# Optimization experiments

Measured on AMD Instinct MI355X. Metric: run time of the kernel, lower is better.

The kernel has to match this reference:

```python
import jax, jax.numpy as jnp
import numpy as np

B, L, D, H = 32, 1024, 1024, 1024

def setup_inputs() -> dict:
    key = jax.random.key(0)
    k1, k2, k3 = jax.random.split(key, 3)
    query = jax.random.normal(k1, (B, L, D), dtype=jnp.float32)
    keys = jax.random.normal(k2, (B, L, D), dtype=jnp.float32)
    # xavier_normal for Linear(D, H): std = sqrt(2/(D+H))
    W = jax.random.normal(k3, (H, D), dtype=jnp.float32) * np.sqrt(2.0 / (D + H)).astype(np.float32)
    b = jnp.zeros((H,), dtype=jnp.float32)
    return {"query": query, "keys": keys, "W": W, "b": b}

def reference(query, keys, W, b):
    # L2-normalize along feature dim (matches torch .norm(dim=-1, keepdim=True))
    qn = query / jnp.linalg.norm(query, axis=-1, keepdims=True)
    kn = keys / jnp.linalg.norm(keys, axis=-1, keepdims=True)
    # scores[b,i,j] = <kn[b,i], qn[b,j]>  ->  [B, Lk, Lq]
    scores = jnp.einsum('bid,bjd->bij', kn, qn)
    attn = jax.nn.softmax(scores, axis=-1)
    # bmm(attn, keys) then sum over batch -> [L, D]
    out = jnp.einsum('bij,bjd->id', attn, keys)
    x = jax.nn.relu(out @ W.T + b)
    return (x, attn)
```

## Files before the change

kernel.cpp:

```cpp
#include <hip/hip_runtime.h>
#include <hip/hip_bf16.h>

#define NBATCH 32
#define Ls 1024
#define Ds 1024
#define Hs 1024

typedef float f32x4 __attribute__((ext_vector_type(4)));
typedef __bf16 v8bf __attribute__((ext_vector_type(8)));
typedef unsigned short u16x8 __attribute__((ext_vector_type(8)));
typedef unsigned short u16x4 __attribute__((ext_vector_type(4)));
typedef __hip_bfloat16 bf16;

__device__ __forceinline__ float bfbits2f(unsigned short h) {
  unsigned u = ((unsigned)h) << 16;
  return __builtin_bit_cast(float, u);
}
__device__ __forceinline__ unsigned short f2b(float x) {
  return __builtin_bit_cast(unsigned short, __float2bfloat16(x));
}
__device__ __forceinline__ u16x8 pack8(const float4& a, const float4& b, float s) {
  u16x8 r;
  r[0] = f2b(a.x * s); r[1] = f2b(a.y * s); r[2] = f2b(a.z * s); r[3] = f2b(a.w * s);
  r[4] = f2b(b.x * s); r[5] = f2b(b.y * s); r[6] = f2b(b.z * s); r[7] = f2b(b.w * s);
  return r;
}

__global__ __launch_bounds__(256) void k_convq(const float* __restrict__ q,
                                               bf16* __restrict__ qn) {
  const int w0 = ((int)blockIdx.x * 256 + (int)threadIdx.x) >> 6;
  const int lane = threadIdx.x & 63;
  #pragma unroll
  for (int it = 0; it < 2; ++it) {
    const size_t r0 = ((size_t)(it * 8192 + w0)) * 2;
    const float4* q0 = reinterpret_cast<const float4*>(q + r0 * Ds);
    float4 qv[2][4];
    #pragma unroll
    for (int rr = 0; rr < 2; ++rr)
      #pragma unroll
      for (int h = 0; h < 2; ++h) {
        qv[rr][h * 2 + 0] = q0[rr * 256 + h * 128 + lane * 2 + 0];
        qv[rr][h * 2 + 1] = q0[rr * 256 + h * 128 + lane * 2 + 1];
      }
    float sq0 = 0.f, sq1 = 0.f;
    #pragma unroll
    for (int p = 0; p < 4; ++p) {
      sq0 += qv[0][p].x*qv[0][p].x + qv[0][p].y*qv[0][p].y + qv[0][p].z*qv[0][p].z + qv[0][p].w*qv[0][p].w;
      sq1 += qv[1][p].x*qv[1][p].x + qv[1][p].y*qv[1][p].y + qv[1][p].z*qv[1][p].z + qv[1][p].w*qv[1][p].w;
    }
    #pragma unroll
    for (int o = 1; o < 64; o <<= 1) { sq0 += __shfl_xor(sq0, o); sq1 += __shfl_xor(sq1, o); }
    const float iq0 = 1.0f / sqrtf(sq0), iq1 = 1.0f / sqrtf(sq1);
    u16x8* qo = reinterpret_cast<u16x8*>(qn + r0 * Ds);
    qo[lane]        = pack8(qv[0][0], qv[0][1], iq0);
    qo[64 + lane]   = pack8(qv[0][2], qv[0][3], iq0);
    qo[128 + lane]  = pack8(qv[1][0], qv[1][1], iq1);
    qo[192 + lane]  = pack8(qv[1][2], qv[1][3], iq1);
  }
}

__global__ __launch_bounds__(256) void k_convkT(const float* __restrict__ k,
                                                bf16* __restrict__ kb,
                                                bf16* __restrict__ kT,
                                                float* __restrict__ invk) {
  __shared__ float tile[64][65];
  __shared__ float red[4][16][16];
  const int b = blockIdx.y;
  const int j0 = blockIdx.x * 64;
  const int t = threadIdx.x;
  const int jr = t >> 4;
  const int cg = t & 15;
  const int c4 = cg * 4;
  const float* src = k + (size_t)b * Ls * Ds + (size_t)j0 * Ds;
  bf16* kbd = kb + (size_t)b * Ls * Ds + (size_t)j0 * Ds;
  bf16* kTd = kT + (size_t)b * Ds * Ls + j0;
  float ssq[4] = {0.f, 0.f, 0.f, 0.f};

  for (int dc = 0; dc < 16; ++dc) {
    const int d0 = dc * 64;
    float4 v[4];
    #pragma unroll
    for (int rr = 0; rr < 4; ++rr) {
      const int j = jr + rr * 16;
      v[rr] = *reinterpret_cast<const float4*>(&src[(size_t)j * Ds + d0 + c4]);
      ssq[rr] += v[rr].x*v[rr].x + v[rr].y*v[rr].y + v[rr].z*v[rr].z + v[rr].w*v[rr].w;
      u16x4 o = { f2b(v[rr].x), f2b(v[rr].y), f2b(v[rr].z), f2b(v[rr].w) };
      *reinterpret_cast<u16x4*>(&kbd[(size_t)j * Ds + d0 + c4]) = o;
    }
    __syncthreads();
    #pragma unroll
    for (int rr = 0; rr < 4; ++rr) {
      const int j = jr + rr * 16;
      tile[j][c4 + 0] = v[rr].x; tile[j][c4 + 1] = v[rr].y;
      tile[j][c4 + 2] = v[rr].z; tile[j][c4 + 3] = v[rr].w;
    }
    __syncthreads();
    #pragma unroll
    for (int rr = 0; rr < 4; ++rr) {
      const int dd = jr + rr * 16;
      u16x4 o = { f2b(tile[c4 + 0][dd]), f2b(tile[c4 + 1][dd]),
                  f2b(tile[c4 + 2][dd]), f2b(tile[c4 + 3][dd]) };
      *reinterpret_cast<u16x4*>(&kTd[(size_t)(d0 + dd) * Ls + c4]) = o;
    }
  }

  #pragma unroll
  for (int rr = 0; rr < 4; ++rr) red[rr][jr][cg] = ssq[rr];
  __syncthreads();
  if (t < 64) {
    const int r = (t & 15) + (t >> 4) * 16;
    float s = 0.f;
    #pragma unroll
    for (int c = 0; c < 16; ++c) s += red[t >> 4][t & 15][c];
    invk[(size_t)b * Ls + j0 + r] = 1.0f / sqrtf(s);
  }
}

__global__ __launch_bounds__(256) void k_w2(const float* __restrict__ W,
                                            bf16* __restrict__ W2) {
  const size_t idx = (size_t)blockIdx.x * 256 + threadIdx.x;
  const size_t e0 = idx * 4;
  const size_t h = e0 >> 10, d = e0 & 1023;
  const float4 w = reinterpret_cast<const float4*>(W)[idx];
  u16x4 wh = { f2b(w.x), f2b(w.y), f2b(w.z), f2b(w.w) };
  u16x4 wl = { f2b(w.x - bfbits2f(wh[0])), f2b(w.y - bfbits2f(wh[1])),
               f2b(w.z - bfbits2f(wh[2])), f2b(w.w - bfbits2f(wh[3])) };
  bf16* row = W2 + h * 3072;
  *reinterpret_cast<u16x4*>(row + d) = wh;
  *reinterpret_cast<u16x4*>(row + 1024 + d) = wh;
  *reinterpret_cast<u16x4*>(row + 2048 + d) = wl;
}

template<int KT, int MODE>
__global__ __launch_bounds__(512) void k_gemm256(
    const bf16* __restrict__ A, const bf16* __restrict__ B,
    void* __restrict__ Cv, const float* __restrict__ scale,
    int lda, int ldb, int ldc, int nb,
    size_t sA, size_t sB, size_t zA, size_t zB, size_t zC, size_t zS)
{
  __shared__ bf16 lds[2][2][256 * 64];
  const int tid = threadIdx.x;
  const int lane = tid & 63;
  const int wid = tid >> 6;
  const int wr = wid >> 2;
  const int wc = wid & 3;
  const size_t m0 = (size_t)blockIdx.y * 256;
  const size_t n0 = (size_t)blockIdx.x * 256;
  const bf16* Az = A + (size_t)blockIdx.z * zA;
  const bf16* Bz = B + (size_t)blockIdx.z * zB;

  const int srow = tid >> 3;
  const int sslot = tid & 7;
  f32x4 acc[8][4] = {};

  auto stage = [&](int tt, int buf) {
    const int b = tt / KT;
    const int k0 = (tt - b * KT) * 64;
    const bf16* Abp = Az + (size_t)b * sA;
    const bf16* Bbp = Bz + (size_t)b * sB;
    #pragma unroll
    for (int c = 0; c < 4; ++c) {
      const int row = c * 64 + srow;
      const int ksl = (sslot ^ (row & 7)) * 8;
      __builtin_amdgcn_global_load_lds(
          (const __attribute__((address_space(1))) void*)(Abp + (m0 + row) * lda + k0 + ksl),
          (__attribute__((address_space(3))) void*)(&lds[buf][0][c * 4096 + tid * 8]), 16, 0, 0);
    }
    #pragma unroll
    for (int c = 0; c < 4; ++c) {
      const int row = c * 64 + srow;
      const int ksl = (sslot ^ (row & 7)) * 8;
      __builtin_amdgcn_global_load_lds(
          (const __attribute__((address_space(1))) void*)(Bbp + (n0 + row) * ldb + k0 + ksl),
          (__attribute__((address_space(3))) void*)(&lds[buf][1][c * 4096 + tid * 8]), 16, 0, 0);
    }
  };

  const int rsel = lane & 15, qd = lane >> 4;
  auto compute = [&](int buf) {
    const bf16* As = lds[buf][0];
    const bf16* Bs = lds[buf][1];
    v8bf bfrag[2][4];
    #pragma unroll
    for (int h = 0; h < 2; ++h)
      #pragma unroll
      for (int n = 0; n < 4; ++n) {
        const int r = wc * 64 + n * 16 + rsel;
        const int s = (h * 4 + qd) ^ (r & 7);
        bfrag[h][n] = *reinterpret_cast<const v8bf*>(
            reinterpret_cast<const char*>(Bs) + r * 128 + s * 16);
      }
    #pragma unroll
    for (int m = 0; m < 8; ++m) {
      const int r = wr * 128 + m * 16 + rsel;
      const int s0 = qd ^ (r & 7);
      const int s1 = (4 + qd) ^ (r & 7);
      const v8bf a0 = *reinterpret_cast<const v8bf*>(
          reinterpret_cast<const char*>(As) + r * 128 + s0 * 16);
      const v8bf a1 = *reinterpret_cast<const v8bf*>(
          reinterpret_cast<const char*>(As) + r * 128 + s1 * 16);
      #pragma unroll
      for (int n = 0; n < 4; ++n)
        acc[m][n] = __builtin_amdgcn_mfma_f32_16x16x32_bf16(a0, bfrag[0][n], acc[m][n], 0, 0, 0);
      #pragma unroll
      for (int n = 0; n < 4; ++n)
        acc[m][n] = __builtin_amdgcn_mfma_f32_16x16x32_bf16(a1, bfrag[1][n], acc[m][n], 0, 0, 0);
    }
  };

  const int T = KT * nb;
  stage(0, 0);
  for (int t = 0; t < T - 1; ++t) {
    __builtin_amdgcn_s_barrier();
    stage(t + 1, (t + 1) & 1);
    asm volatile("s_waitcnt vmcnt(8)" ::: "memory");
    __builtin_amdgcn_s_barrier();
    compute(t & 1);
  }
  asm volatile("s_waitcnt vmcnt(0)" ::: "memory");
  __builtin_amdgcn_s_barrier();
  compute((T - 1) & 1);

  if (MODE == 0) {
    float* Cz = (float*)Cv + (size_t)blockIdx.z * zC;
    #pragma unroll
    for (int m = 0; m < 8; ++m) {
      const size_t ri = m0 + wr * 128 + m * 16 + (size_t)((lane >> 4) * 4);
      #pragma unroll
      for (int n = 0; n < 4; ++n) {
        const size_t cj = n0 + wc * 64 + n * 16 + (lane & 15);
        #pragma unroll
        for (int r = 0; r < 4; ++r)
          Cz[(ri + r) * ldc + cj] = acc[m][n][r];
      }
    }
  } else {
    bf16* Cz = (bf16*)Cv + (size_t)blockIdx.z * zC;
    const float* Sz = scale + (size_t)blockIdx.z * zS;
    #pragma unroll
    for (int m = 0; m < 8; ++m) {
      const size_t ri = m0 + wr * 128 + m * 16 + (size_t)((lane >> 4) * 4);
      const float4 ik = *reinterpret_cast<const float4*>(Sz + ri);
      #pragma unroll
      for (int n = 0; n < 4; ++n) {
        const size_t cj = n0 + wc * 64 + n * 16 + (lane & 15);
        Cz[(ri + 0) * ldc + cj] = __float2bfloat16(acc[m][n][0] * ik.x);
        Cz[(ri + 1) * ldc + cj] = __float2bfloat16(acc[m][n][1] * ik.y);
        Cz[(ri + 2) * ldc + cj] = __float2bfloat16(acc[m][n][2] * ik.z);
        Cz[(ri + 3) * ldc + cj] = __float2bfloat16(acc[m][n][3] * ik.w);
      }
    }
  }
}

__global__ __launch_bounds__(256) void k_gemm_nt(
    const bf16* __restrict__ A, const bf16* __restrict__ B,
    float* __restrict__ C,
    int lda, int ldb, int ldc, int K,
    size_t zA, size_t zB, size_t zC)
{
  __shared__ bf16 As[128 * 32];
  __shared__ bf16 Bs[128 * 32];
  const int tid = threadIdx.x;
  const int lane = tid & 63;
  const int wc = (tid >> 6) & 1;
  const int wr = (tid >> 7) & 1;
  const size_t m0 = (size_t)blockIdx.y * 128;
  const size_t n0 = (size_t)blockIdx.x * 128;
  const bf16* Az = A + (size_t)blockIdx.z * zA;
  const bf16* Bz = B + (size_t)blockIdx.z * zB;
  float* Cz = C + (size_t)blockIdx.z * zC;
  f32x4 acc[4][4] = {};

  const int beta0 = tid * 16;
  const int row0 = tid >> 2;
  const int kk0 = ((tid & 3) ^ ((row0 >> 1) & 3)) * 8;
  const int sw = (((lane >> 4) ^ ((lane >> 1) & 3)) << 4);
  const int rsel = lane & 15;

  for (int k0 = 0; k0 < K; k0 += 32) {
    __syncthreads();
    __builtin_amdgcn_global_load_lds(
        (const __attribute__((address_space(1))) void*)(Az + (m0 + row0) * lda + (k0 + kk0)),
        (__attribute__((address_space(3))) void*)(&As[beta0 / 2]), 16, 0, 0);
    __builtin_amdgcn_global_load_lds(
        (const __attribute__((address_space(1))) void*)(Az + (m0 + row0 + 64) * lda + (k0 + kk0)),
        (__attribute__((address_space(3))) void*)(&As[beta0 / 2 + 2048]), 16, 0, 0);
    __builtin_amdgcn_global_load_lds(
        (const __attribute__((address_space(1))) void*)(Bz + (n0 + row0) * ldb + (k0 + kk0)),
        (__attribute__((address_space(3))) void*)(&Bs[beta0 / 2]), 16, 0, 0);
    __builtin_amdgcn_global_load_lds(
        (const __attribute__((address_space(1))) void*)(Bz + (n0 + row0 + 64) * ldb + (k0 + kk0)),
        (__attribute__((address_space(3))) void*)(&Bs[beta0 / 2 + 2048]), 16, 0, 0);
    __syncthreads();

    v8bf af[4], bg[4];
    #pragma unroll
    for (int m = 0; m < 4; ++m) {
      const int rA = wr * 64 + m * 16 + rsel;
      af[m] = *reinterpret_cast<const v8bf*>(reinterpret_cast<const char*>(As) + rA * 64 + sw);
      const int rB = wc * 64 + m * 16 + rsel;
      bg[m] = *reinterpret_cast<const v8bf*>(reinterpret_cast<const char*>(Bs) + rB * 64 + sw);
    }
    #pragma unroll
    for (int m = 0; m < 4; ++m)
      #pragma unroll
      for (int n = 0; n < 4; ++n)
        acc[m][n] = __builtin_amdgcn_mfma_f32_16x16x32_bf16(af[m], bg[n], acc[m][n], 0, 0, 0);
  }

  #pragma unroll
  for (int m = 0; m < 4; ++m) {
    const size_t ri = m0 + wr * 64 + m * 16 + ((lane >> 4) * 4);
    #pragma unroll
    for (int n = 0; n < 4; ++n) {
      const size_t cj = n0 + wc * 64 + n * 16 + (lane & 15);
      #pragma unroll
      for (int r = 0; r < 4; ++r)
        Cz[(ri + r) * ldc + cj] = acc[m][n][r];
    }
  }
}

__global__ __launch_bounds__(256) void k_softmax(const bf16* __restrict__ sc,
                                                 float* __restrict__ attn,
                                                 bf16* __restrict__ abf) {
  const int wave = ((int)blockIdx.x * 256 + (int)threadIdx.x) >> 6;
  const int lane = threadIdx.x & 63;
  for (int i = 0; i < 4; ++i) {
    const size_t row = (size_t)wave * 4 + i;
    const u16x8* sr = reinterpret_cast<const u16x8*>(sc + row * Ls);
    const u16x8 s0 = sr[lane], s1 = sr[lane + 64];
    float e[16];
    float ss = 0.f;
    #pragma unroll
    for (int j = 0; j < 8; ++j) { e[j] = __expf(bfbits2f(s0[j])); ss += e[j]; }
    #pragma unroll
    for (int j = 0; j < 8; ++j) { e[8 + j] = __expf(bfbits2f(s1[j])); ss += e[8 + j]; }
    #pragma unroll
    for (int o = 1; o < 64; o <<= 1) ss += __shfl_xor(ss, o);
    const float inv = 1.0f / ss;
    #pragma unroll
    for (int j = 0; j < 16; ++j) e[j] *= inv;
    float4* ar = reinterpret_cast<float4*>(attn + row * Ls);
    float4 a0 = {e[0], e[1], e[2], e[3]},   a1 = {e[4], e[5], e[6], e[7]};
    float4 a2 = {e[8], e[9], e[10], e[11]}, a3 = {e[12], e[13], e[14], e[15]};
    ar[lane * 2 + 0] = a0;  ar[lane * 2 + 1] = a1;
    ar[128 + lane * 2 + 0] = a2;  ar[128 + lane * 2 + 1] = a3;
    u16x8* ab8 = reinterpret_cast<u16x8*>(abf + row * Ls);
    u16x8 b0, b1;
    #pragma unroll
    for (int j = 0; j < 8; ++j) { b0[j] = f2b(e[j]); b1[j] = f2b(e[8 + j]); }
    ab8[lane] = b0;
    ab8[64 + lane] = b1;
  }
}

__global__ __launch_bounds__(256) void k_reduce(const float* __restrict__ part,
                                                bf16* __restrict__ A2) {
  const size_t idx = (size_t)blockIdx.x * 256 + threadIdx.x;
  float4 s = {0.f, 0.f, 0.f, 0.f};
  #pragma unroll
  for (int g = 0; g < 16; ++g) {
    const float4 p = reinterpret_cast<const float4*>(part + (size_t)g * (Ls * Ds))[idx];
    s.x += p.x; s.y += p.y; s.z += p.z; s.w += p.w;
  }
  const size_t e0 = idx * 4;
  const size_t i = e0 >> 10, d = e0 & 1023;
  u16x4 h = { f2b(s.x), f2b(s.y), f2b(s.z), f2b(s.w) };
  u16x4 l = { f2b(s.x - bfbits2f(h[0])), f2b(s.y - bfbits2f(h[1])),
              f2b(s.z - bfbits2f(h[2])), f2b(s.w - bfbits2f(h[3])) };
  bf16* row = A2 + i * 3072;
  *reinterpret_cast<u16x4*>(row + d) = h;
  *reinterpret_cast<u16x4*>(row + 1024 + d) = l;
  *reinterpret_cast<u16x4*>(row + 2048 + d) = h;
}

__global__ __launch_bounds__(256) void k_reduce2(const float* __restrict__ part2,
                                                 const float* __restrict__ bias,
                                                 float* __restrict__ xout) {
  const size_t idx = (size_t)blockIdx.x * 256 + threadIdx.x;
  float4 s = {0.f, 0.f, 0.f, 0.f};
  #pragma unroll
  for (int g = 0; g < 4; ++g) {
    const float4 p = reinterpret_cast<const float4*>(part2 + (size_t)g * (Ls * Hs))[idx];
    s.x += p.x; s.y += p.y; s.z += p.z; s.w += p.w;
  }
  const size_t h0 = (idx * 4) & 1023;
  const float4 bv = *reinterpret_cast<const float4*>(bias + h0);
  s.x = fmaxf(s.x + bv.x, 0.f); s.y = fmaxf(s.y + bv.y, 0.f);
  s.z = fmaxf(s.z + bv.z, 0.f); s.w = fmaxf(s.w + bv.w, 0.f);
  reinterpret_cast<float4*>(xout)[idx] = s;
}

extern "C" void kernel_launch(void* const* d_in, const int* in_sizes, int n_in,
                              void* d_out, int out_size, void* d_ws, size_t ws_size,
                              hipStream_t stream) {
  const float* q = (const float*)d_in[0];
  const float* k = (const float*)d_in[1];
  const float* W = (const float*)d_in[2];
  const float* bias = (const float*)d_in[3];
  float* xout = (float*)d_out;
  float* attn = (float*)d_out + (size_t)Ls * Hs;

  char* w = (char*)d_ws;
  bf16* qn    = (bf16*)w;
  bf16* kb    = (bf16*)(w + ((size_t)64 << 20));
  bf16* kT    = (bf16*)(w + ((size_t)128 << 20));
  bf16* sc_bf = (bf16*)(w + ((size_t)192 << 20));
  bf16* W2    = (bf16*)(w + ((size_t)256 << 20));
  bf16* A2    = (bf16*)(w + ((size_t)263 << 20));
  float* invk = (float*)(w + ((size_t)270 << 20));
  float* part  = (float*)kb;
  float* part2 = (float*)kT;
  bf16* abf = qn;

  k_convq<<<2048, 256, 0, stream>>>(q, qn);
  k_convkT<<<dim3(16, NBATCH), 256, 0, stream>>>(k, kb, kT, invk);
  k_w2<<<(Hs * Ds / 4) / 256, 256, 0, stream>>>(W, W2);

  k_gemm256<16, 1><<<dim3(4, 4, NBATCH), 512, 0, stream>>>(kb, qn, sc_bf, invk,
      Ds, Ds, Ls, 1,
      (size_t)Ls * Ds, (size_t)Ls * Ds,
      (size_t)Ls * Ds, (size_t)Ls * Ds, (size_t)Ls * Ls, (size_t)Ls);

  k_softmax<<<2048, 256, 0, stream>>>(sc_bf, attn, abf);

  k_gemm256<16, 0><<<dim3(4, 4, 16), 512, 0, stream>>>(abf, kT, part, nullptr,
      Ls, Ls, Ds, 2,
      (size_t)Ls * Ls, (size_t)Ls * Ds,
      (size_t)2 * Ls * Ls, (size_t)2 * Ls * Ds, (size_t)Ls * Ds, 0);

  k_reduce<<<(Ls * Ds / 4) / 256, 256, 0, stream>>>(part, A2);

  k_gemm_nt<<<dim3(8, 8, 4), 256, 0, stream>>>(A2, W2, part2,
      3072, 3072, Hs, 768, 768, 768, (size_t)Ls * Hs);

  k_reduce2<<<(Ls * Hs / 4) / 256, 256, 0, stream>>>(part2, bias, xout);
}
```

Measured before the change: 357.5 us.

## Interleave chunked global-to-LDS prefetch with MFMA quarters in GEMM main loop

Restructures the bf16 GEMM main loop so that the prefetch for tile t+2 is split into chunks. Each chunk is issued into the current LDS buffer as soon as that buffer's rows have been read into registers, interleaved with four quarter-sized MFMA groups. The MFMA groups are wrapped in s_setprio and separated by barriers and sched_barriers. The goal is to overlap global loads with matrix math and deepen the prefetch beyond simple double-buffering. In exchange there are many more barriers per iteration and register-held fragments, and correctness depends on the exact read-before-overwrite ordering.

```diff
diff --git a/kernel.cpp b/kernel.cpp
--- a/kernel.cpp
+++ b/kernel.cpp
@@ -153,73 +153,104 @@
   const int sslot = tid & 7;
   f32x4 acc[8][4] = {};
 
-  auto stage = [&](int tt, int buf) {
-    const int b = tt / KT;
-    const int k0 = (tt - b * KT) * 64;
-    const bf16* Abp = Az + (size_t)b * sA;
-    const bf16* Bbp = Bz + (size_t)b * sB;
-    #pragma unroll
-    for (int c = 0; c < 4; ++c) {
-      const int row = c * 64 + srow;
-      const int ksl = (sslot ^ (row & 7)) * 8;
-      __builtin_amdgcn_global_load_lds(
-          (const __attribute__((address_space(1))) void*)(Abp + (m0 + row) * lda + k0 + ksl),
-          (__attribute__((address_space(3))) void*)(&lds[buf][0][c * 4096 + tid * 8]), 16, 0, 0);
-    }
-    #pragma unroll
-    for (int c = 0; c < 4; ++c) {
-      const int row = c * 64 + srow;
-      const int ksl = (sslot ^ (row & 7)) * 8;
-      __builtin_amdgcn_global_load_lds(
-          (const __attribute__((address_space(1))) void*)(Bbp + (n0 + row) * ldb + k0 + ksl),
-          (__attribute__((address_space(3))) void*)(&lds[buf][1][c * 4096 + tid * 8]), 16, 0, 0);
-    }
+  auto stageChunk = [&](int tt, int ab, int c, int buf) {
+    const int bz = tt / KT;
+    const int k0 = (tt - bz * KT) * 64;
+    const int row = c * 64 + srow;
+    const int ksl = (sslot ^ (row & 7)) * 8;
+    const bf16* src = (ab == 0)
+        ? (Az + (size_t)bz * sA + (m0 + row) * lda + k0 + ksl)
+        : (Bz + (size_t)bz * sB + (n0 + row) * ldb + k0 + ksl);
+    __builtin_amdgcn_global_load_lds(
+        (const __attribute__((address_space(1))) void*)src,
+        (__attribute__((address_space(3))) void*)(&lds[buf][ab][c * 4096 + tid * 8]), 16, 0, 0);
   };
 
   const int rsel = lane & 15, qd = lane >> 4;
-  auto compute = [&](int buf) {
-    const bf16* As = lds[buf][0];
-    const bf16* Bs = lds[buf][1];
-    v8bf bfrag[2][4];
-    #pragma unroll
-    for (int h = 0; h < 2; ++h)
-      #pragma unroll
-      for (int n = 0; n < 4; ++n) {
-        const int r = wc * 64 + n * 16 + rsel;
+  v8bf a[4][2], b[4][2];
+
+  auto readA = [&](const bf16* As, int mh) {
+    #pragma unroll
+    for (int m = 0; m < 4; ++m) {
+      const int r = wr * 128 + mh * 64 + m * 16 + rsel;
+      #pragma unroll
+      for (int h = 0; h < 2; ++h) {
         const int s = (h * 4 + qd) ^ (r & 7);
-        bfrag[h][n] = *reinterpret_cast<const v8bf*>(
-            reinterpret_cast<const char*>(Bs) + r * 128 + s * 16);
-      }
-    #pragma unroll
-    for (int m = 0; m < 8; ++m) {
-      const int r = wr * 128 + m * 16 + rsel;
-      const int s0 = qd ^ (r & 7);
-      const int s1 = (4 + qd) ^ (r & 7);
-      const v8bf a0 = *reinterpret_cast<const v8bf*>(
-          reinterpret_cast<const char*>(As) + r * 128 + s0 * 16);
-      const v8bf a1 = *reinterpret_cast<const v8bf*>(
-          reinterpret_cast<const char*>(As) + r * 128 + s1 * 16);
-      #pragma unroll
-      for (int n = 0; n < 4; ++n)
-        acc[m][n] = __builtin_amdgcn_mfma_f32_16x16x32_bf16(a0, bfrag[0][n], acc[m][n], 0, 0, 0);
-      #pragma unroll
-      for (int n = 0; n < 4; ++n)
-        acc[m][n] = __builtin_amdgcn_mfma_f32_16x16x32_bf16(a1, bfrag[1][n], acc[m][n], 0, 0, 0);
+        a[m][h] = *reinterpret_cast<const v8bf*>(reinterpret_cast<const char*>(As) + r * 128 + s * 16);
+      }
     }
   };
+  auto readB2 = [&](const bf16* Bs, int npair) {
+    #pragma unroll
+    for (int n = 0; n < 2; ++n) {
+      const int r = wc * 64 + (npair * 2 + n) * 16 + rsel;
+      #pragma unroll
+      for (int h = 0; h < 2; ++h) {
+        const int s = (h * 4 + qd) ^ (r & 7);
+        b[npair * 2 + n][h] = *reinterpret_cast<const v8bf*>(reinterpret_cast<const char*>(Bs) + r * 128 + s * 16);
+      }
+    }
+  };
+  auto mfma8 = [&](int mh, int npair) {
+    __builtin_amdgcn_s_setprio(1);
+    #pragma unroll
+    for (int m = 0; m < 4; ++m)
+      #pragma unroll
+      for (int n = 0; n < 2; ++n) {
+        const int mi = mh * 4 + m, ni = npair * 2 + n;
+        acc[mi][ni] = __builtin_amdgcn_mfma_f32_16x16x32_bf16(a[m][0], b[ni][0], acc[mi][ni], 0, 0, 0);
+        acc[mi][ni] = __builtin_amdgcn_mfma_f32_16x16x32_bf16(a[m][1], b[ni][1], acc[mi][ni], 0, 0, 0);
+      }
+    __builtin_amdgcn_s_setprio(0);
+  };
 
   const int T = KT * nb;
-  stage(0, 0);
-  for (int t = 0; t < T - 1; ++t) {
+
+  #pragma unroll
+  for (int c = 0; c < 4; ++c) stageChunk(0, 0, c, 0);
+  #pragma unroll
+  for (int c = 0; c < 4; ++c) stageChunk(0, 1, c, 0);
+  #pragma unroll
+  for (int c = 0; c < 4; ++c) stageChunk(1, 0, c, 1);
+  #pragma unroll
+  for (int c = 0; c < 4; ++c) stageChunk(1, 1, c, 1);
+  asm volatile("s_waitcnt vmcnt(8)" ::: "memory");
+  __builtin_amdgcn_s_barrier();
+
+  for (int t = 0; t < T; ++t) {
+    const int d = t & 1;
+    const bf16* As = lds[d][0];
+    const bf16* Bs = lds[d][1];
+    const int u = t + 2;
+    const bool st = (u < T);
+
+    readA(As, 0); readB2(Bs, 0);
+    __builtin_amdgcn_s_barrier(); __builtin_amdgcn_sched_barrier(0);
+    mfma8(0, 0);
     __builtin_amdgcn_s_barrier();
-    stage(t + 1, (t + 1) & 1);
-    asm volatile("s_waitcnt vmcnt(8)" ::: "memory");
+
+    readB2(Bs, 1);
+    if (st) { stageChunk(u, 0, 0, d); stageChunk(u, 0, 2, d); }
+    __builtin_amdgcn_s_barrier(); __builtin_amdgcn_sched_barrier(0);
+    mfma8(0, 1);
     __builtin_amdgcn_s_barrier();
-    compute(t & 1);
-  }
-  asm volatile("s_waitcnt vmcnt(0)" ::: "memory");
-  __builtin_amdgcn_s_barrier();
-  compute((T - 1) & 1);
+
+    readA(As, 1);
+    if (st) { stageChunk(u, 1, 0, d); stageChunk(u, 1, 1, d); }
+    __builtin_amdgcn_s_barrier(); __builtin_amdgcn_sched_barrier(0);
+    mfma8(1, 1);
+    __builtin_amdgcn_s_barrier();
+
+    if (st) { stageChunk(u, 0, 1, d); stageChunk(u, 0, 3, d);
+              stageChunk(u, 1, 2, d); stageChunk(u, 1, 3, d); }
+    __builtin_amdgcn_s_barrier(); __builtin_amdgcn_sched_barrier(0);
+    mfma8(1, 0);
+    if (t < T - 1) {
+      if (st) { asm volatile("s_waitcnt vmcnt(8)" ::: "memory"); }
+      else    { asm volatile("s_waitcnt vmcnt(0)" ::: "memory"); }
+      __builtin_amdgcn_s_barrier();
+    }
+  }
 
   if (MODE == 0) {
     float* Cz = (float*)Cv + (size_t)blockIdx.z * zC;
```

Result: faster. 347.1 us (-2.9%).
